# Performance work log

Measured on AMD Instinct MI355X. Metric: run time of the kernel, lower is better.

## Reference

```python
import jax, jax.numpy as jnp
import numpy as np

B, H, S, F_RANK, D_HEAD = 1, 8, 4096, 64, 64
NEG = -1e9


def setup_inputs() -> dict:
    key = jax.random.key(0)
    k1, k2, k3, k4 = jax.random.split(key, 4)
    v = jax.random.normal(k1, (B, H, S, D_HEAD), dtype=jnp.float32)
    A1 = jax.random.normal(k2, (B, H, S, F_RANK), dtype=jnp.float32)
    A2 = jax.random.normal(k3, (B, H, F_RANK, S), dtype=jnp.float32)
    mask = jax.random.randint(k4, (B, 1, S, S), 0, 2, dtype=jnp.int32)
    return {"v": v, "A1": A1, "A2": A2, "mask": mask, "len_q": S}


def reference(v, A1, A2, mask, len_q):
    # Rank-f factorized scores: [B,H,len_q,len_q]
    scores = jnp.einsum('bhsf,bhft->bhst', A1[:, :, :len_q, :], A2[:, :, :, :len_q])
    scores = scores[:mask.shape[0]]
    # masked_fill(mask != 0, -1e9)
    scores = jnp.where(mask[:, :, :len_q, :len_q] != 0, jnp.float32(NEG), scores)
    attn = jax.nn.softmax(scores, axis=-1)  # dropout is identity in eval mode
    output = jnp.einsum('bhst,bhtd->bhsd', attn, v[:, :, :len_q, :])
    return (output, attn)
```

## Files before the change

### kernel.cpp

```cpp
#include <hip/hip_runtime.h>
#include <hip/hip_bf16.h>
#include <stdint.h>

#define S_LEN 4096
#define NHEAD 8
#define L2E   1.44269504088896340736f

typedef __attribute__((ext_vector_type(8))) _Float16 f16x8;
typedef __attribute__((ext_vector_type(4))) float f32x4;
typedef unsigned short u16;
typedef unsigned int   u32;

#define MFMA16F(a,b,c) __builtin_amdgcn_mfma_f32_16x16x32_f16((a),(b),(c),0,0,0)
#define EXP2F(x) __builtin_amdgcn_exp2f((x))

__device__ __forceinline__ void gl_lds16(const void* g, void* l) {
  __builtin_amdgcn_global_load_lds((const __attribute__((address_space(1))) void*)g,
                                   (__attribute__((address_space(3))) void*)l, 16, 0, 0);
}

#define WS_A2F  0u
#define WS_VF   (4u<<20)
#define WS_BM   (8u<<20)
#define WS_INVL (10u<<20)

__global__ void pk_mask(const int* __restrict__ mask, u32* __restrict__ bmT) {
  const int sb = blockIdx.x >> 4;
  const int t  = (blockIdx.x & 15) * 256 + threadIdx.x;
  u32 w = 0;
  #pragma unroll
  for (int j = 0; j < 32; ++j)
    w |= (mask[(size_t)(sb * 32 + j) * S_LEN + t] != 0 ? 1u : 0u) << j;
  bmT[sb * S_LEN + t] = w;
}

__global__ void pk_tsplit16(const float* __restrict__ src, _Float16* __restrict__ dst,
                            int chunk_stride, int row_stride) {
  const int h = blockIdx.x >> 6, ci = blockIdx.x & 63;
  const float* base = src + (size_t)h * (S_LEN * 64) + (size_t)ci * chunk_stride;
  __shared__ float tile[64][65];
  const int jr = threadIdx.x & 63, ir = threadIdx.x >> 6;
  #pragma unroll
  for (int p = 0; p < 16; ++p) {
    int i = p * 4 + ir;
    tile[i][jr] = base[(size_t)i * row_stride + jr];
  }
  __syncthreads();
  const size_t ob = (size_t)(h * 64 + ci) * 4096;
  #pragma unroll
  for (int p = 0; p < 16; ++p) {
    int o = p * 256 + threadIdx.x;
    int r = o >> 6;
    int cc = (o & 63) ^ ((r & 7) << 3);
    dst[ob + o] = (_Float16)tile[cc][r];
  }
}

__device__ __forceinline__ void load_a1(const float* __restrict__ A1, int h, int sbase,
                                        int c, int g, f16x8 (&a1f)[2][2]) {
  #pragma unroll
  for (int mt = 0; mt < 2; ++mt)
    #pragma unroll
    for (int kk = 0; kk < 2; ++kk) {
      const float* p = A1 + ((size_t)(h * S_LEN + sbase + mt * 16 + c) * 64 + kk * 32 + g * 8);
      float4 x0 = ((const float4*)p)[0];
      float4 x1 = ((const float4*)p)[1];
      f16x8 f;
      f[0] = (_Float16)x0.x; f[1] = (_Float16)x0.y; f[2] = (_Float16)x0.z; f[3] = (_Float16)x0.w;
      f[4] = (_Float16)x1.x; f[5] = (_Float16)x1.y; f[6] = (_Float16)x1.z; f[7] = (_Float16)x1.w;
      a1f[mt][kk] = f;
    }
}

__launch_bounds__(256, 2)
__global__ void fattn_pass1(const float* __restrict__ A1, const _Float16* __restrict__ a2f,
                            const u32* __restrict__ bmT,  float* __restrict__ invl) {
  const int h   = blockIdx.x & 7;
  const int sb  = blockIdx.x >> 3;
  const int tid = threadIdx.x;
  const int w = tid >> 6, lane = tid & 63;
  const int g = lane >> 4, c = lane & 15;
  const int wsr = w >> 1;
  const int wth = w & 1;
  const int sbase = sb * 64 + wsr * 32;
  const int sb32  = sb * 2 + wsr;

  __shared__ __align__(16) char smem[16896];
  float* mll = (float*)(smem + 16384);

  f16x8 a1f[2][2];
  load_a1(A1, h, sbase, c, g, a1f);

  float rl[2][4];
  #pragma unroll
  for (int mt = 0; mt < 2; ++mt)
    #pragma unroll
    for (int r = 0; r < 4; ++r) rl[mt][r] = 0.f;

  const u32* bmrow = bmT + (size_t)sb32 * S_LEN;

  auto stage2 = [&](int bufi, int ci) {
    const size_t tb = (size_t)(h * 64 + ci) * 4096;
    char* lb = smem + bufi * 8192;
    #pragma unroll
    for (int i = 0; i < 2; ++i) {
      const int off = i * 4096 + tid * 16;
      gl_lds16((const char*)(a2f + tb) + off, lb + off);
    }
  };

  stage2(0, 0);
  __syncthreads();

  #pragma unroll 1
  for (int ci = 0; ci < 64; ++ci) {
    if (ci < 63) stage2((ci + 1) & 1, ci + 1);

    const _Float16* base = (const _Float16*)(smem + (ci & 1) * 8192);

    f32x4 acc[2][2];
    #pragma unroll
    for (int mt = 0; mt < 2; ++mt)
      #pragma unroll
      for (int nt = 0; nt < 2; ++nt) acc[mt][nt] = (f32x4){0.f, 0.f, 0.f, 0.f};
    #pragma unroll
    for (int kk = 0; kk < 2; ++kk)
      #pragma unroll
      for (int nt = 0; nt < 2; ++nt) {
        int eb = (wth * 32 + nt * 16 + c) * 64 + ((kk * 32 + g * 8) ^ ((c & 7) << 3));
        f16x8 bh = *(const f16x8*)(base + eb);
        #pragma unroll
        for (int mt = 0; mt < 2; ++mt)
          acc[mt][nt] = MFMA16F(a1f[mt][kk], bh, acc[mt][nt]);
      }

    const u32 mw0 = bmrow[ci * 64 + wth * 32 + c];
    const u32 mw1 = bmrow[ci * 64 + wth * 32 + 16 + c];
    #pragma unroll
    for (int mt = 0; mt < 2; ++mt)
      #pragma unroll
      for (int nt = 0; nt < 2; ++nt) {
        const u32 mwv = nt ? mw1 : mw0;
        #pragma unroll
        for (int r = 0; r < 4; ++r) {
          float ex = EXP2F(acc[mt][nt][r] * L2E);
          rl[mt][r] += ((mwv >> (mt * 16 + g * 4 + r)) & 1u) ? 0.f : ex;
        }
      }

    __syncthreads();
  }

  #pragma unroll
  for (int mt = 0; mt < 2; ++mt)
    #pragma unroll
    for (int r = 0; r < 4; ++r) {
      float s = rl[mt][r];
      #pragma unroll
      for (int off = 1; off < 16; off <<= 1) s += __shfl_xor(s, off);
      rl[mt][r] = s;
    }
  __syncthreads();
  if (c == 0) {
    #pragma unroll
    for (int mt = 0; mt < 2; ++mt)
      #pragma unroll
      for (int r = 0; r < 4; ++r)
        mll[w * 32 + mt * 16 + g * 4 + r] = rl[mt][r];
  }
  __syncthreads();
  if (wth == 0 && c == 0) {
    #pragma unroll
    for (int mt = 0; mt < 2; ++mt)
      #pragma unroll
      for (int r = 0; r < 4; ++r) {
        float tot = rl[mt][r] + mll[(w ^ 1) * 32 + mt * 16 + g * 4 + r];
        invl[h * S_LEN + sbase + mt * 16 + g * 4 + r] = 1.0f / tot;
      }
  }
}

__launch_bounds__(256, 2)
__global__ void fattn_pass2(const float* __restrict__ A1, const _Float16* __restrict__ a2f,
                            const _Float16* __restrict__ vf, const u32* __restrict__ bmT,
                            const float* __restrict__ invl, float* __restrict__ dout) {
  const int h   = blockIdx.x & 7;
  const int sb  = blockIdx.x >> 3;
  const int tid = threadIdx.x;
  const int w = tid >> 6, lane = tid & 63;
  const int g = lane >> 4, c = lane & 15;
  const int wsr = w >> 1;
  const int wth = w & 1;
  const int sbase = sb * 64 + wsr * 32;
  const int sb32  = sb * 2 + wsr;

  __shared__ __align__(16) char smem[43008];
  _Float16* atb = (_Float16*)(smem + 32768);

  f16x8 a1f[2][2];
  load_a1(A1, h, sbase, c, g, a1f);

  float inv[2][4];
  #pragma unroll
  for (int mt = 0; mt < 2; ++mt)
    #pragma unroll
    for (int r = 0; r < 4; ++r)
      inv[mt][r] = invl[h * S_LEN + sbase + mt * 16 + g * 4 + r];

  f32x4 oacc[2][4];
  #pragma unroll
  for (int mt = 0; mt < 2; ++mt)
    #pragma unroll
    for (int dt = 0; dt < 4; ++dt) oacc[mt][dt] = (f32x4){0.f, 0.f, 0.f, 0.f};

  const u32* bmrow = bmT + (size_t)sb32 * S_LEN;
  float* aout = dout + (size_t)NHEAD * S_LEN * 64;
  _Float16* myatb = atb + w * 1280;

  auto stage_all = [&](int bufi, int ci) {
    const size_t tb = (size_t)(h * 64 + ci) * 4096;
    char* lb = smem + bufi * 16384;
    #pragma unroll
    for (int i = 0; i < 2; ++i) {
      const int off = i * 4096 + tid * 16;
      gl_lds16((const char*)(a2f + tb) + off, lb +        off);
      gl_lds16((const char*)(vf  + tb) + off, lb + 8192 + off);
    }
  };

  stage_all(0, 0);
  __syncthreads();

  #pragma unroll 1
  for (int ci = 0; ci < 64; ++ci) {
    if (ci < 63) stage_all((ci + 1) & 1, ci + 1);

    const _Float16* base = (const _Float16*)(smem + (ci & 1) * 16384);

    f32x4 acc[2][2];
    #pragma unroll
    for (int mt = 0; mt < 2; ++mt)
      #pragma unroll
      for (int nt = 0; nt < 2; ++nt) acc[mt][nt] = (f32x4){0.f, 0.f, 0.f, 0.f};
    #pragma unroll
    for (int kk = 0; kk < 2; ++kk)
      #pragma unroll
      for (int nt = 0; nt < 2; ++nt) {
        int eb = (wth * 32 + nt * 16 + c) * 64 + ((kk * 32 + g * 8) ^ ((c & 7) << 3));
        f16x8 bh = *(const f16x8*)(base + eb);
        #pragma unroll
        for (int mt = 0; mt < 2; ++mt)
          acc[mt][nt] = MFMA16F(a1f[mt][kk], bh, acc[mt][nt]);
      }

    const u32 mw0 = bmrow[ci * 64 + wth * 32 + c];
    const u32 mw1 = bmrow[ci * 64 + wth * 32 + 16 + c];
    float av[2][2][4];
    #pragma unroll
    for (int mt = 0; mt < 2; ++mt)
      #pragma unroll
      for (int nt = 0; nt < 2; ++nt) {
        const u32 mwv = nt ? mw1 : mw0;
        #pragma unroll
        for (int r = 0; r < 4; ++r) {
          float ex = EXP2F(acc[mt][nt][r] * L2E);
          av[mt][nt][r] = ((mwv >> (mt * 16 + g * 4 + r)) & 1u) ? 0.f : ex * inv[mt][r];
        }
      }

    #pragma unroll
    for (int mt = 0; mt < 2; ++mt)
      #pragma unroll
      for (int nt = 0; nt < 2; ++nt)
        #pragma unroll
        for (int r = 0; r < 4; ++r)
          myatb[(mt * 16 + g * 4 + r) * 40 + nt * 16 + c] = (_Float16)av[mt][nt][r];

    asm volatile("" ::: "memory");

    f16x8 af[2];
    #pragma unroll
    for (int mt = 0; mt < 2; ++mt)
      af[mt] = *(const f16x8*)(myatb + (mt * 16 + c) * 40 + g * 8);

    {
      const size_t rb = (size_t)(h * S_LEN + sbase) * S_LEN + ci * 64 + wth * 32;
      #pragma unroll
      for (int mt = 0; mt < 2; ++mt)
        #pragma unroll
        for (int nt = 0; nt < 2; ++nt)
          #pragma unroll
          for (int r = 0; r < 4; ++r)
            aout[rb + (size_t)(mt * 16 + g * 4 + r) * S_LEN + nt * 16 + c] = av[mt][nt][r];
    }

    #pragma unroll
    for (int dt = 0; dt < 4; ++dt) {
      int ve = (dt * 16 + c) * 64 + ((wth * 32 + g * 8) ^ ((c & 7) << 3));
      f16x8 bv = *(const f16x8*)(base + 4096 + ve);
      #pragma unroll
      for (int mt = 0; mt < 2; ++mt)
        oacc[mt][dt] = MFMA16F(af[mt], bv, oacc[mt][dt]);
    }

    __syncthreads();
  }

  __syncthreads();
  float* outx = (float*)smem;
  if (wth == 1) {
    #pragma unroll
    for (int mt = 0; mt < 2; ++mt)
      #pragma unroll
      for (int dt = 0; dt < 4; ++dt)
        #pragma unroll
        for (int r = 0; r < 4; ++r)
          outx[wsr * 2112 + (mt * 16 + g * 4 + r) * 66 + dt * 16 + c] = oacc[mt][dt][r];
  }
  __syncthreads();
  if (wth == 0) {
    #pragma unroll
    for (int mt = 0; mt < 2; ++mt)
      #pragma unroll
      for (int dt = 0; dt < 4; ++dt)
        #pragma unroll
        for (int r = 0; r < 4; ++r) {
          float vv = oacc[mt][dt][r] + outx[wsr * 2112 + (mt * 16 + g * 4 + r) * 66 + dt * 16 + c];
          int s = sbase + mt * 16 + g * 4 + r;
          dout[(size_t)(h * S_LEN + s) * 64 + dt * 16 + c] = vv;
        }
  }
}

extern "C" void kernel_launch(void* const* d_in, const int* in_sizes, int n_in,
                              void* d_out, int out_size, void* d_ws, size_t ws_size,
                              hipStream_t stream) {
  (void)in_sizes; (void)n_in; (void)out_size; (void)ws_size;
  const float* v    = (const float*)d_in[0];
  const float* A1   = (const float*)d_in[1];
  const float* A2   = (const float*)d_in[2];
  const int*   mask = (const int*)d_in[3];
  float* out = (float*)d_out;
  char* ws = (char*)d_ws;

  _Float16* a2f = (_Float16*)(ws + WS_A2F);
  _Float16* vf  = (_Float16*)(ws + WS_VF);
  u32* bmT      = (u32*)(ws + WS_BM);
  float* invl   = (float*)(ws + WS_INVL);

  pk_mask    <<<2048, 256, 0, stream>>>(mask, bmT);
  pk_tsplit16<<<512,  256, 0, stream>>>(A2, a2f, 64, 4096);
  pk_tsplit16<<<512,  256, 0, stream>>>(v,  vf,  4096, 64);
  fattn_pass1<<<512, 256, 0, stream>>>(A1, a2f, bmT, invl);
  fattn_pass2<<<512, 256, 0, stream>>>(A1, a2f, vf, bmT, invl, out);
}
```

Measured before the change: 730.4 us.

## Fuse softmax normalizer pass into output pass with smaller row tiles

Merges the two attention kernels into one block that first computes row sums over all key chunks and then recomputes scores to write the normalized attention and the output. The invl round trip and one launch go away. Each block now covers 32 query rows instead of 64, giving 1024 blocks and a launch bound of 4 blocks per SM for more parallelism. In exchange, each A2 tile is reused by fewer rows, so global/L2 traffic for A2 and V per row doubles. The mask bitmap is indexed by sb with a per-wave bit offset.

```diff
diff --git a/kernel.cpp b/kernel.cpp
--- a/kernel.cpp
+++ b/kernel.cpp
@@ -22,7 +22,6 @@
 #define WS_A2F  0u
 #define WS_VF   (4u<<20)
 #define WS_BM   (8u<<20)
-#define WS_INVL (10u<<20)
 
 __global__ void pk_mask(const int* __restrict__ mask, u32* __restrict__ bmT) {
   const int sb = blockIdx.x >> 4;
@@ -56,25 +55,10 @@
   }
 }
 
-__device__ __forceinline__ void load_a1(const float* __restrict__ A1, int h, int sbase,
-                                        int c, int g, f16x8 (&a1f)[2][2]) {
-  #pragma unroll
-  for (int mt = 0; mt < 2; ++mt)
-    #pragma unroll
-    for (int kk = 0; kk < 2; ++kk) {
-      const float* p = A1 + ((size_t)(h * S_LEN + sbase + mt * 16 + c) * 64 + kk * 32 + g * 8);
-      float4 x0 = ((const float4*)p)[0];
-      float4 x1 = ((const float4*)p)[1];
-      f16x8 f;
-      f[0] = (_Float16)x0.x; f[1] = (_Float16)x0.y; f[2] = (_Float16)x0.z; f[3] = (_Float16)x0.w;
-      f[4] = (_Float16)x1.x; f[5] = (_Float16)x1.y; f[6] = (_Float16)x1.z; f[7] = (_Float16)x1.w;
-      a1f[mt][kk] = f;
-    }
-}
-
-__launch_bounds__(256, 2)
-__global__ void fattn_pass1(const float* __restrict__ A1, const _Float16* __restrict__ a2f,
-                            const u32* __restrict__ bmT,  float* __restrict__ invl) {
+__launch_bounds__(256, 4)
+__global__ void fattn_fused(const float* __restrict__ A1, const _Float16* __restrict__ a2f,
+                            const _Float16* __restrict__ vf, const u32* __restrict__ bmT,
+                            float* __restrict__ dout) {
   const int h   = blockIdx.x & 7;
   const int sb  = blockIdx.x >> 3;
   const int tid = threadIdx.x;
@@ -82,225 +66,161 @@
   const int g = lane >> 4, c = lane & 15;
   const int wsr = w >> 1;
   const int wth = w & 1;
-  const int sbase = sb * 64 + wsr * 32;
-  const int sb32  = sb * 2 + wsr;
-
-  __shared__ __align__(16) char smem[16896];
-  float* mll = (float*)(smem + 16384);
-
-  f16x8 a1f[2][2];
-  load_a1(A1, h, sbase, c, g, a1f);
-
-  float rl[2][4];
-  #pragma unroll
-  for (int mt = 0; mt < 2; ++mt)
-    #pragma unroll
-    for (int r = 0; r < 4; ++r) rl[mt][r] = 0.f;
-
-  const u32* bmrow = bmT + (size_t)sb32 * S_LEN;
-
-  auto stage2 = [&](int bufi, int ci) {
+  const int sbase = sb * 32 + wsr * 16;
+
+  __shared__ __align__(16) char smem[38400];
+  _Float16* atb = (_Float16*)(smem + 32768);
+  float*    mll = (float*)(smem + 37888);
+
+  f16x8 a1f[2];
+  #pragma unroll
+  for (int kk = 0; kk < 2; ++kk) {
+    const float* p = A1 + ((size_t)(h * S_LEN + sbase + c) * 64 + kk * 32 + g * 8);
+    float4 x0 = ((const float4*)p)[0];
+    float4 x1 = ((const float4*)p)[1];
+    f16x8 f;
+    f[0] = (_Float16)x0.x; f[1] = (_Float16)x0.y; f[2] = (_Float16)x0.z; f[3] = (_Float16)x0.w;
+    f[4] = (_Float16)x1.x; f[5] = (_Float16)x1.y; f[6] = (_Float16)x1.z; f[7] = (_Float16)x1.w;
+    a1f[kk] = f;
+  }
+
+  const u32* bmrow = bmT + (size_t)sb * S_LEN;
+  const int mbit = wsr * 16;
+
+  auto stage_a2 = [&](int bufi, int ci) {
     const size_t tb = (size_t)(h * 64 + ci) * 4096;
-    char* lb = smem + bufi * 8192;
+    char* lb = smem + bufi * 16384;
     #pragma unroll
     for (int i = 0; i < 2; ++i) {
       const int off = i * 4096 + tid * 16;
       gl_lds16((const char*)(a2f + tb) + off, lb + off);
     }
   };
-
-  stage2(0, 0);
-  __syncthreads();
-
-  #pragma unroll 1
-  for (int ci = 0; ci < 64; ++ci) {
-    if (ci < 63) stage2((ci + 1) & 1, ci + 1);
-
-    const _Float16* base = (const _Float16*)(smem + (ci & 1) * 8192);
-
-    f32x4 acc[2][2];
-    #pragma unroll
-    for (int mt = 0; mt < 2; ++mt)
-      #pragma unroll
-      for (int nt = 0; nt < 2; ++nt) acc[mt][nt] = (f32x4){0.f, 0.f, 0.f, 0.f};
+  auto stage_v = [&](int bufi, int ci) {
+    const size_t tb = (size_t)(h * 64 + ci) * 4096;
+    char* lb = smem + bufi * 16384 + 8192;
+    #pragma unroll
+    for (int i = 0; i < 2; ++i) {
+      const int off = i * 4096 + tid * 16;
+      gl_lds16((const char*)(vf + tb) + off, lb + off);
+    }
+  };
+
+  auto scores = [&](const _Float16* base, f32x4 (&acc)[2]) {
+    #pragma unroll
+    for (int nt = 0; nt < 2; ++nt) acc[nt] = (f32x4){0.f, 0.f, 0.f, 0.f};
     #pragma unroll
     for (int kk = 0; kk < 2; ++kk)
       #pragma unroll
       for (int nt = 0; nt < 2; ++nt) {
         int eb = (wth * 32 + nt * 16 + c) * 64 + ((kk * 32 + g * 8) ^ ((c & 7) << 3));
         f16x8 bh = *(const f16x8*)(base + eb);
-        #pragma unroll
-        for (int mt = 0; mt < 2; ++mt)
-          acc[mt][nt] = MFMA16F(a1f[mt][kk], bh, acc[mt][nt]);
-      }
+        acc[nt] = MFMA16F(a1f[kk], bh, acc[nt]);
+      }
+  };
+
+  float rl[4] = {0.f, 0.f, 0.f, 0.f};
+
+  stage_a2(0, 0);
+  __syncthreads();
+
+  #pragma unroll 1
+  for (int ci = 0; ci < 64; ++ci) {
+    if (ci < 63) stage_a2((ci + 1) & 1, ci + 1);
+
+    const _Float16* base = (const _Float16*)(smem + (ci & 1) * 16384);
+    f32x4 acc[2];
+    scores(base, acc);
 
     const u32 mw0 = bmrow[ci * 64 + wth * 32 + c];
     const u32 mw1 = bmrow[ci * 64 + wth * 32 + 16 + c];
     #pragma unroll
-    for (int mt = 0; mt < 2; ++mt)
-      #pragma unroll
-      for (int nt = 0; nt < 2; ++nt) {
-        const u32 mwv = nt ? mw1 : mw0;
-        #pragma unroll
-        for (int r = 0; r < 4; ++r) {
-          float ex = EXP2F(acc[mt][nt][r] * L2E);
-          rl[mt][r] += ((mwv >> (mt * 16 + g * 4 + r)) & 1u) ? 0.f : ex;
-        }
-      }
-
+    for (int nt = 0; nt < 2; ++nt) {
+      const u32 mwv = nt ? mw1 : mw0;
+      #pragma unroll
+      for (int r = 0; r < 4; ++r) {
+        float ex = EXP2F(acc[nt][r] * L2E);
+        rl[r] += ((mwv >> (mbit + g * 4 + r)) & 1u) ? 0.f : ex;
+      }
+    }
     __syncthreads();
   }
 
   #pragma unroll
-  for (int mt = 0; mt < 2; ++mt)
-    #pragma unroll
-    for (int r = 0; r < 4; ++r) {
-      float s = rl[mt][r];
-      #pragma unroll
-      for (int off = 1; off < 16; off <<= 1) s += __shfl_xor(s, off);
-      rl[mt][r] = s;
-    }
+  for (int r = 0; r < 4; ++r) {
+    float s = rl[r];
+    #pragma unroll
+    for (int off = 1; off < 16; off <<= 1) s += __shfl_xor(s, off);
+    rl[r] = s;
+  }
   __syncthreads();
   if (c == 0) {
     #pragma unroll
-    for (int mt = 0; mt < 2; ++mt)
-      #pragma unroll
-      for (int r = 0; r < 4; ++r)
-        mll[w * 32 + mt * 16 + g * 4 + r] = rl[mt][r];
-  }
-  __syncthreads();
-  if (wth == 0 && c == 0) {
-    #pragma unroll
-    for (int mt = 0; mt < 2; ++mt)
-      #pragma unroll
-      for (int r = 0; r < 4; ++r) {
-        float tot = rl[mt][r] + mll[(w ^ 1) * 32 + mt * 16 + g * 4 + r];
-        invl[h * S_LEN + sbase + mt * 16 + g * 4 + r] = 1.0f / tot;
-      }
-  }
-}
-
-__launch_bounds__(256, 2)
-__global__ void fattn_pass2(const float* __restrict__ A1, const _Float16* __restrict__ a2f,
-                            const _Float16* __restrict__ vf, const u32* __restrict__ bmT,
-                            const float* __restrict__ invl, float* __restrict__ dout) {
-  const int h   = blockIdx.x & 7;
-  const int sb  = blockIdx.x >> 3;
-  const int tid = threadIdx.x;
-  const int w = tid >> 6, lane = tid & 63;
-  const int g = lane >> 4, c = lane & 15;
-  const int wsr = w >> 1;
-  const int wth = w & 1;
-  const int sbase = sb * 64 + wsr * 32;
-  const int sb32  = sb * 2 + wsr;
-
-  __shared__ __align__(16) char smem[43008];
-  _Float16* atb = (_Float16*)(smem + 32768);
-
-  f16x8 a1f[2][2];
-  load_a1(A1, h, sbase, c, g, a1f);
-
-  float inv[2][4];
-  #pragma unroll
-  for (int mt = 0; mt < 2; ++mt)
-    #pragma unroll
-    for (int r = 0; r < 4; ++r)
-      inv[mt][r] = invl[h * S_LEN + sbase + mt * 16 + g * 4 + r];
-
-  f32x4 oacc[2][4];
-  #pragma unroll
-  for (int mt = 0; mt < 2; ++mt)
-    #pragma unroll
-    for (int dt = 0; dt < 4; ++dt) oacc[mt][dt] = (f32x4){0.f, 0.f, 0.f, 0.f};
-
-  const u32* bmrow = bmT + (size_t)sb32 * S_LEN;
+    for (int r = 0; r < 4; ++r) mll[w * 16 + g * 4 + r] = rl[r];
+  }
+  __syncthreads();
+  float inv[4];
+  #pragma unroll
+  for (int r = 0; r < 4; ++r)
+    inv[r] = 1.0f / (rl[r] + mll[(w ^ 1) * 16 + g * 4 + r]);
+
+  f32x4 oacc[4];
+  #pragma unroll
+  for (int dt = 0; dt < 4; ++dt) oacc[dt] = (f32x4){0.f, 0.f, 0.f, 0.f};
+
   float* aout = dout + (size_t)NHEAD * S_LEN * 64;
-  _Float16* myatb = atb + w * 1280;
-
-  auto stage_all = [&](int bufi, int ci) {
-    const size_t tb = (size_t)(h * 64 + ci) * 4096;
-    char* lb = smem + bufi * 16384;
-    #pragma unroll
-    for (int i = 0; i < 2; ++i) {
-      const int off = i * 4096 + tid * 16;
-      gl_lds16((const char*)(a2f + tb) + off, lb +        off);
-      gl_lds16((const char*)(vf  + tb) + off, lb + 8192 + off);
-    }
-  };
-
-  stage_all(0, 0);
+  _Float16* myatb = atb + w * 640;
+
+  __syncthreads();
+  stage_a2(0, 0);
+  stage_v(0, 0);
   __syncthreads();
 
   #pragma unroll 1
   for (int ci = 0; ci < 64; ++ci) {
-    if (ci < 63) stage_all((ci + 1) & 1, ci + 1);
+    if (ci < 63) { stage_a2((ci + 1) & 1, ci + 1); stage_v((ci + 1) & 1, ci + 1); }
 
     const _Float16* base = (const _Float16*)(smem + (ci & 1) * 16384);
-
-    f32x4 acc[2][2];
-    #pragma unroll
-    for (int mt = 0; mt < 2; ++mt)
-      #pragma unroll
-      for (int nt = 0; nt < 2; ++nt) acc[mt][nt] = (f32x4){0.f, 0.f, 0.f, 0.f};
-    #pragma unroll
-    for (int kk = 0; kk < 2; ++kk)
-      #pragma unroll
-      for (int nt = 0; nt < 2; ++nt) {
-        int eb = (wth * 32 + nt * 16 + c) * 64 + ((kk * 32 + g * 8) ^ ((c & 7) << 3));
-        f16x8 bh = *(const f16x8*)(base + eb);
-        #pragma unroll
-        for (int mt = 0; mt < 2; ++mt)
-          acc[mt][nt] = MFMA16F(a1f[mt][kk], bh, acc[mt][nt]);
-      }
+    f32x4 acc[2];
+    scores(base, acc);
 
     const u32 mw0 = bmrow[ci * 64 + wth * 32 + c];
     const u32 mw1 = bmrow[ci * 64 + wth * 32 + 16 + c];
-    float av[2][2][4];
-    #pragma unroll
-    for (int mt = 0; mt < 2; ++mt)
-      #pragma unroll
-      for (int nt = 0; nt < 2; ++nt) {
-        const u32 mwv = nt ? mw1 : mw0;
-        #pragma unroll
-        for (int r = 0; r < 4; ++r) {
-          float ex = EXP2F(acc[mt][nt][r] * L2E);
-          av[mt][nt][r] = ((mwv >> (mt * 16 + g * 4 + r)) & 1u) ? 0.f : ex * inv[mt][r];
-        }
-      }
-
-    #pragma unroll
-    for (int mt = 0; mt < 2; ++mt)
+    float av[2][4];
+    #pragma unroll
+    for (int nt = 0; nt < 2; ++nt) {
+      const u32 mwv = nt ? mw1 : mw0;
+      #pragma unroll
+      for (int r = 0; r < 4; ++r) {
+        float ex = EXP2F(acc[nt][r] * L2E);
+        av[nt][r] = ((mwv >> (mbit + g * 4 + r)) & 1u) ? 0.f : ex * inv[r];
+      }
+    }
+
+    #pragma unroll
+    for (int nt = 0; nt < 2; ++nt)
+      #pragma unroll
+      for (int r = 0; r < 4; ++r)
+        myatb[(g * 4 + r) * 40 + nt * 16 + c] = (_Float16)av[nt][r];
+
+    asm volatile("" ::: "memory");
+
+    f16x8 af = *(const f16x8*)(myatb + c * 40 + g * 8);
+
+    {
+      const size_t rb = (size_t)(h * S_LEN + sbase) * S_LEN + ci * 64 + wth * 32;
       #pragma unroll
       for (int nt = 0; nt < 2; ++nt)
         #pragma unroll
         for (int r = 0; r < 4; ++r)
-          myatb[(mt * 16 + g * 4 + r) * 40 + nt * 16 + c] = (_Float16)av[mt][nt][r];
-
-    asm volatile("" ::: "memory");
-
-    f16x8 af[2];
-    #pragma unroll
-    for (int mt = 0; mt < 2; ++mt)
-      af[mt] = *(const f16x8*)(myatb + (mt * 16 + c) * 40 + g * 8);
-
-    {
-      const size_t rb = (size_t)(h * S_LEN + sbase) * S_LEN + ci * 64 + wth * 32;
-      #pragma unroll
-      for (int mt = 0; mt < 2; ++mt)
-        #pragma unroll
-        for (int nt = 0; nt < 2; ++nt)
-          #pragma unroll
-          for (int r = 0; r < 4; ++r)
-            aout[rb + (size_t)(mt * 16 + g * 4 + r) * S_LEN + nt * 16 + c] = av[mt][nt][r];
+          aout[rb + (size_t)(g * 4 + r) * S_LEN + nt * 16 + c] = av[nt][r];
     }
 
     #pragma unroll
     for (int dt = 0; dt < 4; ++dt) {
-      int ve = (dt * 16 + c) * 64 + ((wth * 32 + g * 8) ^ ((c & 7) << 3));
-      f16x8 bv = *(const f16x8*)(base + 4096 + ve);
-      #pragma unroll
-      for (int mt = 0; mt < 2; ++mt)
-        oacc[mt][dt] = MFMA16F(af[mt], bv, oacc[mt][dt]);
+      int ve = 4096 + (dt * 16 + c) * 64 + ((wth * 32 + g * 8) ^ ((c & 7) << 3));
+      f16x8 bv = *(const f16x8*)(base + ve);
+      oacc[dt] = MFMA16F(af, bv, oacc[dt]);
     }
 
     __syncthreads();
@@ -310,25 +230,21 @@
   float* outx = (float*)smem;
   if (wth == 1) {
     #pragma unroll
-    for (int mt = 0; mt < 2; ++mt)
-      #pragma unroll
-      for (int dt = 0; dt < 4; ++dt)
-        #pragma unroll
-        for (int r = 0; r < 4; ++r)
-          outx[wsr * 2112 + (mt * 16 + g * 4 + r) * 66 + dt * 16 + c] = oacc[mt][dt][r];
+    for (int dt = 0; dt < 4; ++dt)
+      #pragma unroll
+      for (int r = 0; r < 4; ++r)
+        outx[wsr * 1056 + (g * 4 + r) * 66 + dt * 16 + c] = oacc[dt][r];
   }
   __syncthreads();
   if (wth == 0) {
     #pragma unroll
-    for (int mt = 0; mt < 2; ++mt)
-      #pragma unroll
-      for (int dt = 0; dt < 4; ++dt)
-        #pragma unroll
-        for (int r = 0; r < 4; ++r) {
-          float vv = oacc[mt][dt][r] + outx[wsr * 2112 + (mt * 16 + g * 4 + r) * 66 + dt * 16 + c];
-          int s = sbase + mt * 16 + g * 4 + r;
-          dout[(size_t)(h * S_LEN + s) * 64 + dt * 16 + c] = vv;
-        }
+    for (int dt = 0; dt < 4; ++dt)
+      #pragma unroll
+      for (int r = 0; r < 4; ++r) {
+        float vv = oacc[dt][r] + outx[wsr * 1056 + (g * 4 + r) * 66 + dt * 16 + c];
+        int s = sbase + g * 4 + r;
+        dout[(size_t)(h * S_LEN + s) * 64 + dt * 16 + c] = vv;
+      }
   }
 }
 
@@ -346,11 +262,9 @@
   _Float16* a2f = (_Float16*)(ws + WS_A2F);
   _Float16* vf  = (_Float16*)(ws + WS_VF);
   u32* bmT      = (u32*)(ws + WS_BM);
-  float* invl   = (float*)(ws + WS_INVL);
 
   pk_mask    <<<2048, 256, 0, stream>>>(mask, bmT);
   pk_tsplit16<<<512,  256, 0, stream>>>(A2, a2f, 64, 4096);
   pk_tsplit16<<<512,  256, 0, stream>>>(v,  vf,  4096, 64);
-  fattn_pass1<<<512, 256, 0, stream>>>(A1, a2f, bmT, invl);
-  fattn_pass2<<<512, 256, 0, stream>>>(A1, a2f, vf, bmT, invl, out);
-}
+  fattn_fused<<<1024, 256, 0, stream>>>(A1, a2f, vf, bmT, out);
+}
```

Result: faster. 699.0 us (-4.3%).
